# Optimization experiments

Hardware: AMD Instinct MI355X
Metric: run time of the kernel (lower is better)

Reference implementation:

```python
import jax, jax.numpy as jnp
import numpy as np
from jax import lax

B = 8            # IMAGES_PER_GPU
A = 261888       # num_anchors (1024x1024 Mask R-CNN FPN anchors)
PRE_NMS_LIMIT = 6000
PROPOSAL_COUNT = 1000
NMS_THRESHOLD = 0.7


def setup_inputs() -> dict:
    key = jax.random.key(0)
    k1, k2, k3, k4 = jax.random.split(key, 4)
    rpn_probs = jax.random.uniform(k1, (B, A, 2), dtype=jnp.float32)
    rpn_bbox = jax.random.normal(k2, (B, A, 4), dtype=jnp.float32)
    # valid normalized anchors: y1,x1 in [0,0.9], height/width in [0.01,0.1]
    yx = jax.random.uniform(k3, (B, A, 2), minval=0.0, maxval=0.9)
    hw = jax.random.uniform(k4, (B, A, 2), minval=0.01, maxval=0.1)
    anchors = jnp.concatenate([yx, yx + hw], axis=-1)  # (y1, x1, y2, x2)
    return {"rpn_probs": rpn_probs, "rpn_bbox": rpn_bbox, "anchors": anchors}


def _apply_box_deltas(boxes, deltas):
    # boxes, deltas: [..., 4] in (y1, x1, y2, x2) / (dy, dx, log(dh), log(dw))
    h = boxes[..., 2] - boxes[..., 0]
    w = boxes[..., 3] - boxes[..., 1]
    cy = boxes[..., 0] + 0.5 * h + deltas[..., 0] * h
    cx = boxes[..., 1] + 0.5 * w + deltas[..., 1] * w
    h = h * jnp.exp(deltas[..., 2])
    w = w * jnp.exp(deltas[..., 3])
    y1 = cy - 0.5 * h
    x1 = cx - 0.5 * w
    return jnp.stack([y1, x1, y1 + h, x1 + w], axis=-1)


def _nms_single(boxes, scores):
    # boxes: [K, 4] already sorted by score descending; greedy NMS, zero-padded
    areas = (boxes[:, 2] - boxes[:, 0]) * (boxes[:, 3] - boxes[:, 1])

    def step(valid, _):
        idx = jnp.argmax(valid)          # first still-valid = highest score
        has = valid[idx]                 # False when no candidates remain
        box = boxes[idx]
        yy1 = jnp.maximum(box[0], boxes[:, 0])
        xx1 = jnp.maximum(box[1], boxes[:, 1])
        yy2 = jnp.minimum(box[2], boxes[:, 2])
        xx2 = jnp.minimum(box[3], boxes[:, 3])
        inter = jnp.maximum(yy2 - yy1, 0.0) * jnp.maximum(xx2 - xx1, 0.0)
        union = (box[2] - box[0]) * (box[3] - box[1]) + areas - inter
        iou = lax.stop_gradient(jnp.where(union > 0, inter / union, 0.0))
        valid = valid & (iou <= NMS_THRESHOLD)  # also suppresses idx (self IoU = 1)
        return valid, jnp.where(has, box, jnp.zeros_like(box))

    _, selected = lax.scan(step, jnp.ones(boxes.shape[0], dtype=bool), None,
                           length=PROPOSAL_COUNT)
    return selected  # [PROPOSAL_COUNT, 4], zero-padded like tf.pad in original


def reference(rpn_probs, rpn_bbox, anchors):
    std = jnp.asarray([0.1, 0.1, 0.2, 0.2], dtype=rpn_bbox.dtype)  # RPN_BBOX_STD_DEV
    scores = rpn_probs[:, :, 1]                 # fg prob [B, A]
    deltas = rpn_bbox * std
    k = min(PRE_NMS_LIMIT, anchors.shape[1])
    top_scores, ix = lax.top_k(scores, k)       # sorted descending, [B, K]
    idx = ix[..., None]
    deltas_k = jnp.take_along_axis(deltas, idx, axis=1)    # [B, K, 4]
    anchors_k = jnp.take_along_axis(anchors, idx, axis=1)  # [B, K, 4]
    boxes = jnp.clip(_apply_box_deltas(anchors_k, deltas_k), 0.0, 1.0)  # window [0,0,1,1]
    return jax.vmap(_nms_single)(boxes, top_scores)  # [B, PROPOSAL_COUNT, 4]
```

## Files before the change

kernel.cpp:

```cpp
#include <hip/hip_runtime.h>
#include <math.h>
#include <stdint.h>

typedef uint32_t u32; typedef uint64_t u64; typedef uint16_t u16; typedef int32_t i32;

#define BATCH 8
#define NA    261888
#define SEGS  32
#define SEGCHUNK 8184
#define WCHUNK 2046
#define SUBCAP 64
#define NSUB  128
#define TOPK  6000
#define PROP  1000
#define TOP1  1024
#define TMPCAP 2048
#define CACHEB 8192
#define FBMAX 16384
#define NW64  16
#define PSTATIC 0x3F7C0000u

#define OFF_FBK   0
#define OFF_CACHE 1048576
#define OFF_CNT   1572864
#define OFF_STAT  1576960
#define OFF_BOX   1577216
#define OFF_AREA  1708288
#define OFF_MASK  1741056
#define WS_NEEDED 2789632


__device__ __forceinline__ void decode_box(const float4 an, const float4 dl,
                                           float4& bx, float& ar) {
    float d0 = __fmul_rn(dl.x, 0.1f), d1 = __fmul_rn(dl.y, 0.1f);
    float d2 = __fmul_rn(dl.z, 0.2f), d3 = __fmul_rn(dl.w, 0.2f);
    float h = __fsub_rn(an.z, an.x), w = __fsub_rn(an.w, an.y);
    float cy = __fadd_rn(__fadd_rn(an.x, __fmul_rn(0.5f, h)), __fmul_rn(d0, h));
    float cx = __fadd_rn(__fadd_rn(an.y, __fmul_rn(0.5f, w)), __fmul_rn(d1, w));
    float h2 = __fmul_rn(h, (float)exp((double)d2));
    float w2 = __fmul_rn(w, (float)exp((double)d3));
    float y1 = __fsub_rn(cy, __fmul_rn(0.5f, h2));
    float x1 = __fsub_rn(cx, __fmul_rn(0.5f, w2));
    float y2 = __fadd_rn(y1, h2);
    float x2 = __fadd_rn(x1, w2);
    y1 = fminf(fmaxf(y1, 0.f), 1.f); x1 = fminf(fmaxf(x1, 0.f), 1.f);
    y2 = fminf(fmaxf(y2, 0.f), 1.f); x2 = fminf(fmaxf(x2, 0.f), 1.f);
    bx = make_float4(y1, x1, y2, x2);
    ar = __fmul_rn(__fsub_rn(y2, y1), __fsub_rn(x2, x1));
}

__device__ __forceinline__ bool sup_pred(const float4 bi, const float ai,
                                         const float4 bj, const float aj) {
    const double tmid = (double)0.7f + 0x1p-25;
    float yy1 = fmaxf(bi.x, bj.x), xx1 = fmaxf(bi.y, bj.y);
    float yy2 = fminf(bi.z, bj.z), xx2 = fminf(bi.w, bj.w);
    float ih = fmaxf(__fsub_rn(yy2, yy1), 0.f);
    float iw = fmaxf(__fsub_rn(xx2, xx1), 0.f);
    float inter = __fmul_rn(ih, iw);
    float uni = __fsub_rn(__fadd_rn(ai, aj), inter);
    return (uni > 0.f) && ((double)inter >= tmid * (double)uni);
}

__global__ __launch_bounds__(256) void k_histcache(const float4* __restrict__ p4,
                                                   u64* __restrict__ cache,
                                                   u32* __restrict__ cnt) {
    const int b = blockIdx.y, seg = blockIdx.x;
    const int wave = threadIdx.x >> 6, lane = threadIdx.x & 63;
    const u64 lmask = (1ull << lane) - 1ull;
    const size_t fbase = ((size_t)b * NA + seg * SEGCHUNK + wave * WCHUNK) >> 1;
    const u32 abase = (u32)(seg * SEGCHUNK + wave * WCHUNK);
    u64* cseg = cache + (size_t)b * CACHEB + (seg * 4 + wave) * SUBCAP;
    u32 wOff = 0;
    #pragma unroll 4
    for (int it = 0; it < 16; ++it) {
        int f = it * 64 + lane;
        bool ok = f < (WCHUNK / 2);
        u32 bitsA = 0, bitsB = 0;
        if (ok) {
            float4 v = p4[fbase + f];
            bitsA = __float_as_uint(v.y);
            bitsB = __float_as_uint(v.w);
        }
        bool pA = ok && bitsA >= PSTATIC;
        bool pB = ok && bitsB >= PSTATIC;
        u64 mA = __ballot(pA);
        u64 mB = __ballot(pB);
        u32 cA = (u32)__popcll(mA);
        if (pA) {
            u32 slot = wOff + (u32)__popcll(mA & lmask);
            if (slot < SUBCAP) cseg[slot] = ((u64)(~bitsA) << 32) | (u64)(abase + 2 * f);
        }
        if (pB) {
            u32 slot = wOff + cA + (u32)__popcll(mB & lmask);
            if (slot < SUBCAP) cseg[slot] = ((u64)(~bitsB) << 32) | (u64)(abase + 2 * f + 1);
        }
        wOff += cA + (u32)__popcll(mB);
    }
    if (lane == 0) cnt[b * NSUB + seg * 4 + wave] = wOff;
}

__global__ __launch_bounds__(1024) void k_sortdec(const u64* __restrict__ cache,
                                                  const u32* __restrict__ cnt,
                                                  const float4* __restrict__ anchors,
                                                  const float4* __restrict__ bbox,
                                                  u32* __restrict__ stat_g,
                                                  float4* __restrict__ boxes,
                                                  float* __restrict__ areas) {
    __shared__ u32 hist[4096];
    __shared__ u32 suffix[4096];
    __shared__ u32 ps[256];
    __shared__ u32 psS[257];
    __shared__ u64 tmp[TMPCAP];
    __shared__ u32 scnt[NSUB];
    __shared__ u32 wq[4];
    __shared__ u32 sP, sN, sBin, stat;
    const int b = blockIdx.x;
    const int tid = threadIdx.x;
    const int lane = tid & 63, wv = tid >> 6;
    if (tid == 0) { stat = 1u; sBin = 0xFFFFFFFFu; }
    for (int i = tid; i < 4096; i += 1024) hist[i] = 0;
    __syncthreads();
    if (tid < NSUB) {
        u32 raw = cnt[b * NSUB + tid];
        scnt[tid] = raw > SUBCAP ? SUBCAP : raw;
        if (raw > SUBCAP) stat = 0u;
    }
    __syncthreads();
    for (int t = tid; t < CACHEB; t += 1024) {
        int sub = t >> 6, off = t & (SUBCAP - 1);
        if (off < (int)scnt[sub]) {
            u32 bits = ~((u32)(cache[(size_t)b * CACHEB + t] >> 32));
            atomicAdd(&hist[(bits >> 6) & 0xFFFu], 1u);
        }
    }
    __syncthreads();
    if (tid < 256) {
        u32 su = 0;
        #pragma unroll
        for (int k = 0; k < 16; ++k) su += hist[tid * 16 + k];
        ps[tid] = su;
    }
    __syncthreads();
    {
        u32 v = (tid < 256) ? ps[tid] : 0u;
        #pragma unroll
        for (int d = 1; d < 64; d <<= 1) {
            u32 o = __shfl_down(v, d);
            if (lane + d < 64) v += o;
        }
        if (tid < 256 && lane == 0) wq[wv] = v;
        __syncthreads();
        if (tid < 256) {
            u32 add = 0;
            for (int q = wv + 1; q < 4; ++q) add += wq[q];
            psS[tid] = v + add;
        }
        if (tid == 0) psS[256] = 0u;
        __syncthreads();
    }
    {
        const int t4 = tid * 4;
        const int seg = tid >> 2;
        const int segEnd = seg * 16 + 15;
        u32 tail = 0;
        for (int bb = t4 + 4; bb <= segEnd; ++bb) tail += hist[bb];
        u32 h0 = hist[t4], h1 = hist[t4 + 1], h2 = hist[t4 + 2], h3 = hist[t4 + 3];
        u32 s3 = psS[seg + 1] + tail;
        u32 s2 = s3 + h3;
        u32 s1 = s2 + h2;
        u32 s0 = s1 + h1;
        suffix[t4] = s0; suffix[t4 + 1] = s1; suffix[t4 + 2] = s2; suffix[t4 + 3] = s3;
        if (s0 < TOP1 && s0 + h0 >= TOP1) sBin = (u32)t4;
        if (s1 < TOP1 && s1 + h1 >= TOP1) sBin = (u32)(t4 + 1);
        if (s2 < TOP1 && s2 + h2 >= TOP1) sBin = (u32)(t4 + 2);
        if (s3 < TOP1 && s3 + h3 >= TOP1) sBin = (u32)(t4 + 3);
    }
    __syncthreads();
    if (tid == 0) {
        if (sBin == 0xFFFFFFFFu) stat = 0u;
        else {
            sP = PSTATIC + (sBin << 6);
            u32 n = suffix[sBin] + hist[sBin];
            sN = n;
            if (n > TMPCAP) stat = 0u;
        }
    }
    __syncthreads();
    if (stat) {
        for (int i = tid; i < 4096; i += 1024) hist[i] = 0;
        __syncthreads();
        const u32 P = sP;
        for (int t = tid; t < CACHEB; t += 1024) {
            int sub = t >> 6, off = t & (SUBCAP - 1);
            if (off < (int)scnt[sub]) {
                u64 key = cache[(size_t)b * CACHEB + t];
                u32 bits = ~((u32)(key >> 32));
                if (bits >= P) {
                    u32 bin = (bits >> 6) & 0xFFFu;
                    u32 arr = atomicAdd(&hist[bin], 1u);
                    tmp[suffix[bin] + arr] = key;
                }
            }
        }
        __syncthreads();
        const u32 n = sN;
        for (u32 t = (u32)tid; t < n; t += 1024) {
            u64 key = tmp[t];
            u32 bits = ~((u32)(key >> 32));
            u32 bin = (bits >> 6) & 0xFFFu;
            u32 base = suffix[bin], len = hist[bin];
            u32 pos = base;
            for (u32 q = base; q < base + len; ++q) pos += (tmp[q] < key) ? 1u : 0u;
            if (pos < TOP1) {
                u32 idx = (u32)key;
                float4 bx; float ar;
                decode_box(anchors[(size_t)b * NA + idx], bbox[(size_t)b * NA + idx], bx, ar);
                boxes[b * TOP1 + pos] = bx;
                areas[b * TOP1 + pos] = ar;
            }
        }
    }
    if (tid == 0) stat_g[b] = stat;
}

__global__ __launch_bounds__(256) void k_mask(const float4* __restrict__ boxes,
                                              const float* __restrict__ areas,
                                              u32* __restrict__ mw32) {
    const int b = blockIdx.y;
    const int wave = threadIdx.x >> 6, lane = threadIdx.x & 63;
    const int irow = blockIdx.x * 4 + wave;
    const int cmax = irow >> 6;
    u32* mt = mw32 + (size_t)b * (NW64 * TOP1 * 2);
    float4 bi = boxes[b * TOP1 + irow];
    float  ai = areas[b * TOP1 + irow];
    u32 myw = 0;
    for (int c = 0; c <= cmax; ++c) {
        float4 bj = boxes[b * TOP1 + c * 64 + lane];
        float  aj = areas[b * TOP1 + c * 64 + lane];
        u64 word = __ballot(sup_pred(bi, ai, bj, aj));
        if (lane == 2 * c)     myw = (u32)word;
        if (lane == 2 * c + 1) myw = (u32)(word >> 32);
    }
    if (lane < 2 * (cmax + 1))
        mt[((lane >> 1) << 11) + (irow << 1) + (lane & 1)] = myw;
}

__global__ __launch_bounds__(1024, 4) void k_nms(const u64* __restrict__ mw_all,
                                                 const float4* __restrict__ boxes,
                                                 const float2* __restrict__ p2,
                                                 const float4* __restrict__ bbox,
                                                 const float4* __restrict__ anchors,
                                                 const u32* __restrict__ stat_g,
                                                 u64* __restrict__ fbkeys,
                                                 float4* __restrict__ out) {
    __shared__ u64 ldsV[NW64];
    __shared__ u32 wpre[NW64 + 1];
    __shared__ u32 sVt;
    const int b = blockIdx.x;
    const int tid = threadIdx.x;
    const int wave = tid >> 6, lane = tid & 63;
    if (wave == 0) {
        const u64* mw = mw_all + (size_t)b * (NW64 * TOP1);
        const u64 lmask = (1ull << lane) - 1ull;
        u64 V[NW64];
        #pragma unroll
        for (int c = 0; c < NW64; ++c) {
            const int i = (c << 6) + lane;
            u64 ext = 0;
            #pragma unroll
            for (int w = 0; w < c; ++w)
                ext |= mw[(w << 10) + i] & V[w];
            const u64 intern = mw[(c << 10) + i] & lmask;
            const bool extSup = (ext != 0ull);
            u64 v = ~0ull;
            for (int it = 0; it < 64; ++it) {
                bool alive = (!extSup) && ((intern & v) == 0ull);
                u64 nv = __ballot(alive);
                if (nv == v) break;
                v = nv;
            }
            V[c] = v;
        }
        if (lane == 0) {
            u32 r = 0;
            #pragma unroll
            for (int c = 0; c < NW64; ++c) { ldsV[c] = V[c]; wpre[c] = r; r += (u32)__popcll(V[c]); }
            wpre[NW64] = r; sVt = r;
        }
    }
    __syncthreads();
    const u32 Vt = sVt;
    if (Vt >= PROP && stat_g[b] != 0u) {
        const int i = tid;
        const int w = i >> 6, bit = i & 63;
        u64 vw = ldsV[w];
        bool isv = ((vw >> bit) & 1ull) != 0ull;
        u32 rank = wpre[w] + (u32)__popcll(vw & ((1ull << bit) - 1ull));
        if (isv && rank < PROP) out[b * PROP + rank] = boxes[b * TOP1 + i];
        return;
    }
    const int i = tid;
    __shared__ float4 abox[PROP];
    __shared__ float  aar[PROP];
    __shared__ u32 fh[4096];
    __shared__ u32 fps[256];
    __shared__ u32 nsh, sP6;
    if (i == 0) nsh = 0;
    for (int z = i; z < 4096; z += 1024) fh[z] = 0;
    __syncthreads();
    for (int a = i; a < NA; a += 1024) {
        u32 bits = __float_as_uint(p2[(size_t)b * NA + a].y);
        atomicAdd(&fh[bits >> 18], 1u);
    }
    __syncthreads();
    if (i < 256) {
        u32 su = 0;
        for (int k = 0; k < 16; ++k) su += fh[i * 16 + k];
        fps[i] = su;
    }
    __syncthreads();
    if (i == 0) {
        u32 acc = 0; int seg = 0;
        for (int t = 255; t >= 0; --t) { if (acc + fps[t] >= TOPK) { seg = t; break; } acc += fps[t]; }
        int b6 = seg * 16; u32 g6 = acc;
        for (int k = 15; k >= 0; --k) {
            u32 c = fh[seg * 16 + k];
            if (g6 + c >= TOPK) { b6 = seg * 16 + k; break; }
            g6 += c;
        }
        sP6 = (u32)b6 << 18;
    }
    __syncthreads();
    u32 P6 = sP6;
    for (int a = i; a < NA; a += 1024) {
        u32 bits = __float_as_uint(p2[(size_t)b * NA + a].y);
        if (bits >= P6) {
            u32 p = atomicAdd(&nsh, 1u);
            if (p < FBMAX) fbkeys[(size_t)b * FBMAX + p] = ((u64)(~bits) << 32) | (u64)a;
        }
    }
    __syncthreads();
    u32 n = nsh; if (n > FBMAX) n = FBMAX;
    volatile u64* vk = (volatile u64*)(fbkeys + (size_t)b * FBMAX);
    for (int i2 = (int)n + i; i2 < FBMAX; i2 += 1024) vk[i2] = ~0ull;
    __syncthreads();
    for (int k = 2; k <= FBMAX; k <<= 1) {
        for (int j = k >> 1; j > 0; j >>= 1) {
            for (int p = i; p < FBMAX / 2; p += 1024) {
                int ii = ((p & ~(j - 1)) << 1) | (p & (j - 1));
                int l = ii | j;
                u64 a = vk[ii], c = vk[l];
                bool up = ((ii & k) == 0);
                if ((a > c) == up) { vk[ii] = c; vk[l] = a; }
            }
            __syncthreads();
        }
    }
    int acc_n = 0;
    int limit = (int)n < TOPK ? (int)n : TOPK;
    for (int t = 0; t < limit && acc_n < PROP; ++t) {
        u32 idx = (u32)vk[t];
        float4 bi2; float ai2;
        decode_box(anchors[(size_t)b * NA + idx], bbox[(size_t)b * NA + idx], bi2, ai2);
        int pred = 0;
        if (i < acc_n) pred = sup_pred(bi2, ai2, abox[i], aar[i]) ? 1 : 0;
        int any = __syncthreads_or(pred);
        if (!any) {
            if (i == 0) {
                abox[acc_n] = bi2; aar[acc_n] = ai2;
                out[b * PROP + acc_n] = bi2;
            }
            ++acc_n;
            __syncthreads();
        }
    }
    for (int t = acc_n + i; t < PROP; t += 1024)
        out[b * PROP + t] = make_float4(0.f, 0.f, 0.f, 0.f);
}


extern "C" void kernel_launch(void* const* d_in, const int* in_sizes, int n_in,
                              void* d_out, int out_size, void* d_ws, size_t ws_size,
                              hipStream_t stream) {
    (void)in_sizes; (void)n_in; (void)out_size;
    if (ws_size < (size_t)WS_NEEDED) return;
    const float2* p2      = (const float2*)d_in[0];
    const float4* p4      = (const float4*)d_in[0];
    const float4* bbox    = (const float4*)d_in[1];
    const float4* anchors = (const float4*)d_in[2];
    float4* out = (float4*)d_out;

    char* ws = (char*)d_ws;
    u64* fbkeys  = (u64*)(ws + OFF_FBK);
    u64* cache   = (u64*)(ws + OFF_CACHE);
    u32* cnt     = (u32*)(ws + OFF_CNT);
    u32* stat_g  = (u32*)(ws + OFF_STAT);
    float4* boxes= (float4*)(ws + OFF_BOX);
    float* areas = (float*)(ws + OFF_AREA);
    u32* mw32    = (u32*)(ws + OFF_MASK);
    u64* mw64    = (u64*)(ws + OFF_MASK);

    dim3 ghc(SEGS, BATCH), gmask(TOP1 / 4, BATCH);
    k_histcache<<<ghc,   256, 0, stream>>>(p4, cache, cnt);
    k_sortdec  <<<BATCH, 1024, 0, stream>>>(cache, cnt, anchors, bbox, stat_g, boxes, areas);
    k_mask     <<<gmask, 256, 0, stream>>>(boxes, areas, mw32);
    k_nms      <<<BATCH, 1024, 0, stream>>>(mw64, boxes, p2, bbox, anchors, stat_g, fbkeys, out);
}
```

Before: 141.6 us.

## Fuse IoU mask and NMS kernels via last-block-done atomic counter

Merges the suppression-mask kernel and the greedy NMS kernel into one launch. Each 1024-thread block computes 16 mask rows, then increments a per-image atomic counter, and the last block to finish per image runs the NMS. This removes one kernel launch and the gap between launches. In exchange it adds threadfence and atomic synchronisation, plus a reset of the counter in the first kernel. It also fully unrolls the histogram loop.

Measured after the change: 164.1 us. 1.16x slower.

```diff
diff --git a/kernel.cpp b/kernel.cpp
--- a/kernel.cpp
+++ b/kernel.cpp
@@ -18,12 +18,14 @@
 #define CACHEB 8192
 #define FBMAX 16384
 #define NW64  16
+#define MBLK  64
 #define PSTATIC 0x3F7C0000u
 
 #define OFF_FBK   0
 #define OFF_CACHE 1048576
 #define OFF_CNT   1572864
 #define OFF_STAT  1576960
+#define OFF_DONE  1577088
 #define OFF_BOX   1577216
 #define OFF_AREA  1708288
 #define OFF_MASK  1741056
@@ -63,15 +65,17 @@
 
 __global__ __launch_bounds__(256) void k_histcache(const float4* __restrict__ p4,
                                                    u64* __restrict__ cache,
-                                                   u32* __restrict__ cnt) {
+                                                   u32* __restrict__ cnt,
+                                                   u32* __restrict__ done) {
     const int b = blockIdx.y, seg = blockIdx.x;
     const int wave = threadIdx.x >> 6, lane = threadIdx.x & 63;
+    if (seg == 0 && b == 0 && threadIdx.x < BATCH) done[threadIdx.x] = 0;
     const u64 lmask = (1ull << lane) - 1ull;
     const size_t fbase = ((size_t)b * NA + seg * SEGCHUNK + wave * WCHUNK) >> 1;
     const u32 abase = (u32)(seg * SEGCHUNK + wave * WCHUNK);
     u64* cseg = cache + (size_t)b * CACHEB + (seg * 4 + wave) * SUBCAP;
     u32 wOff = 0;
-    #pragma unroll 4
+    #pragma unroll
     for (int it = 0; it < 16; ++it) {
         int f = it * 64 + lane;
         bool ok = f < (WCHUNK / 2);
@@ -223,44 +227,51 @@
     if (tid == 0) stat_g[b] = stat;
 }
 
-__global__ __launch_bounds__(256) void k_mask(const float4* __restrict__ boxes,
-                                              const float* __restrict__ areas,
-                                              u32* __restrict__ mw32) {
-    const int b = blockIdx.y;
-    const int wave = threadIdx.x >> 6, lane = threadIdx.x & 63;
-    const int irow = blockIdx.x * 4 + wave;
-    const int cmax = irow >> 6;
-    u32* mt = mw32 + (size_t)b * (NW64 * TOP1 * 2);
-    float4 bi = boxes[b * TOP1 + irow];
-    float  ai = areas[b * TOP1 + irow];
-    u32 myw = 0;
-    for (int c = 0; c <= cmax; ++c) {
-        float4 bj = boxes[b * TOP1 + c * 64 + lane];
-        float  aj = areas[b * TOP1 + c * 64 + lane];
-        u64 word = __ballot(sup_pred(bi, ai, bj, aj));
-        if (lane == 2 * c)     myw = (u32)word;
-        if (lane == 2 * c + 1) myw = (u32)(word >> 32);
-    }
-    if (lane < 2 * (cmax + 1))
-        mt[((lane >> 1) << 11) + (irow << 1) + (lane & 1)] = myw;
-}
-
-__global__ __launch_bounds__(1024, 4) void k_nms(const u64* __restrict__ mw_all,
-                                                 const float4* __restrict__ boxes,
-                                                 const float2* __restrict__ p2,
-                                                 const float4* __restrict__ bbox,
-                                                 const float4* __restrict__ anchors,
-                                                 const u32* __restrict__ stat_g,
-                                                 u64* __restrict__ fbkeys,
-                                                 float4* __restrict__ out) {
+__global__ __launch_bounds__(1024) void k_masknms(const float4* __restrict__ boxes,
+                                                  const float* __restrict__ areas,
+                                                  const float2* __restrict__ p2,
+                                                  const float4* __restrict__ bbox,
+                                                  const float4* __restrict__ anchors,
+                                                  const u32* __restrict__ stat_g,
+                                                  u32* __restrict__ done,
+                                                  u32* __restrict__ mw32,
+                                                  const u64* __restrict__ mw64,
+                                                  u64* __restrict__ fbkeys,
+                                                  float4* __restrict__ out) {
     __shared__ u64 ldsV[NW64];
     __shared__ u32 wpre[NW64 + 1];
-    __shared__ u32 sVt;
-    const int b = blockIdx.x;
+    __shared__ u32 sWin, sVt;
+    const int b = blockIdx.y;
     const int tid = threadIdx.x;
     const int wave = tid >> 6, lane = tid & 63;
+    {
+        const int irow = blockIdx.x * 16 + wave;
+        const int cmax = irow >> 6;
+        u32* mt = mw32 + (size_t)b * (NW64 * TOP1 * 2);
+        float4 bi = boxes[b * TOP1 + irow];
+        float  ai = areas[b * TOP1 + irow];
+        u32 myw = 0;
+        for (int c = 0; c <= cmax; ++c) {
+            float4 bj = boxes[b * TOP1 + c * 64 + lane];
+            float  aj = areas[b * TOP1 + c * 64 + lane];
+            u64 word = __ballot(sup_pred(bi, ai, bj, aj));
+            if (lane == 2 * c)     myw = (u32)word;
+            if (lane == 2 * c + 1) myw = (u32)(word >> 32);
+        }
+        if (lane < 2 * (cmax + 1))
+            mt[((lane >> 1) << 11) + (irow << 1) + (lane & 1)] = myw;
+    }
+    __syncthreads();
+    if (tid == 0) {
+        __threadfence();
+        u32 old = atomicAdd(&done[b], 1u);
+        sWin = (old == (u32)(MBLK - 1)) ? 1u : 0u;
+    }
+    __syncthreads();
+    if (!sWin) return;
+    __threadfence();
     if (wave == 0) {
-        const u64* mw = mw_all + (size_t)b * (NW64 * TOP1);
+        const u64* mw = mw64 + (size_t)b * (NW64 * TOP1);
         const u64 lmask = (1ull << lane) - 1ull;
         u64 V[NW64];
         #pragma unroll
@@ -395,14 +406,14 @@
     u64* cache   = (u64*)(ws + OFF_CACHE);
     u32* cnt     = (u32*)(ws + OFF_CNT);
     u32* stat_g  = (u32*)(ws + OFF_STAT);
+    u32* done    = (u32*)(ws + OFF_DONE);
     float4* boxes= (float4*)(ws + OFF_BOX);
     float* areas = (float*)(ws + OFF_AREA);
     u32* mw32    = (u32*)(ws + OFF_MASK);
     u64* mw64    = (u64*)(ws + OFF_MASK);
 
-    dim3 ghc(SEGS, BATCH), gmask(TOP1 / 4, BATCH);
-    k_histcache<<<ghc,   256, 0, stream>>>(p4, cache, cnt);
+    dim3 ghc(SEGS, BATCH), gmn(MBLK, BATCH);
+    k_histcache<<<ghc,   256, 0, stream>>>(p4, cache, cnt, done);
     k_sortdec  <<<BATCH, 1024, 0, stream>>>(cache, cnt, anchors, bbox, stat_g, boxes, areas);
-    k_mask     <<<gmask, 256, 0, stream>>>(boxes, areas, mw32);
-    k_nms      <<<BATCH, 1024, 0, stream>>>(mw64, boxes, p2, bbox, anchors, stat_g, fbkeys, out);
-}
+    k_masknms  <<<gmn,  1024, 0, stream>>>(boxes, areas, p2, bbox, anchors, stat_g, done, mw32, mw64, fbkeys, out);
+}
```

## Spread NMS bitmask resolution across all 16 waves with per-chunk barriers

Applied to the files above, without the earlier changes.

The serial single-wave greedy NMS over 16 chunks of 64 candidates is split so that each wave owns one 64-row chunk. Each wave preloads its suppression-mask rows into registers up front and accumulates external suppression as earlier chunks finalise, with a block barrier between chunks. This removes the 120 dependent global loads on one wave's critical path, at the cost of 16 block-wide syncs. The histogram loop is also fully unrolled.

Result: faster. 135.6 us, median of 2 (-4.2%).

```diff
diff --git a/kernel.cpp b/kernel.cpp
--- a/kernel.cpp
+++ b/kernel.cpp
@@ -71,7 +71,7 @@
     const u32 abase = (u32)(seg * SEGCHUNK + wave * WCHUNK);
     u64* cseg = cache + (size_t)b * CACHEB + (seg * 4 + wave) * SUBCAP;
     u32 wOff = 0;
-    #pragma unroll 4
+    #pragma unroll
     for (int it = 0; it < 16; ++it) {
         int f = it * 64 + lane;
         bool ok = f < (WCHUNK / 2);
@@ -255,41 +255,47 @@
                                                  float4* __restrict__ out) {
     __shared__ u64 ldsV[NW64];
     __shared__ u32 wpre[NW64 + 1];
-    __shared__ u32 sVt;
     const int b = blockIdx.x;
     const int tid = threadIdx.x;
     const int wave = tid >> 6, lane = tid & 63;
-    if (wave == 0) {
+    {
         const u64* mw = mw_all + (size_t)b * (NW64 * TOP1);
         const u64 lmask = (1ull << lane) - 1ull;
-        u64 V[NW64];
+        u64 rr[NW64];
+        u64 intern = 0;
         #pragma unroll
-        for (int c = 0; c < NW64; ++c) {
-            const int i = (c << 6) + lane;
-            u64 ext = 0;
-            #pragma unroll
-            for (int w = 0; w < c; ++w)
-                ext |= mw[(w << 10) + i] & V[w];
-            const u64 intern = mw[(c << 10) + i] & lmask;
-            const bool extSup = (ext != 0ull);
-            u64 v = ~0ull;
-            for (int it = 0; it < 64; ++it) {
-                bool alive = (!extSup) && ((intern & v) == 0ull);
-                u64 nv = __ballot(alive);
-                if (nv == v) break;
-                v = nv;
+        for (int w = 0; w < NW64; ++w) {
+            u64 v = 0;
+            if (w <= wave) v = mw[(w << 10) + (wave << 6) + lane];
+            if (w == wave) intern = v & lmask;
+            rr[w] = (w < wave) ? v : 0ull;
+        }
+        u64 ext = 0;
+        #pragma unroll
+        for (int s = 0; s < NW64; ++s) {
+            if (wave == s) {
+                const bool extSup = (ext != 0ull);
+                u64 v = ~0ull;
+                for (int it = 0; it < 64; ++it) {
+                    bool alive = (!extSup) && ((intern & v) == 0ull);
+                    u64 nv = __ballot(alive);
+                    if (nv == v) break;
+                    v = nv;
+                }
+                if (lane == 0) ldsV[s] = v;
             }
-            V[c] = v;
-        }
-        if (lane == 0) {
-            u32 r = 0;
-            #pragma unroll
-            for (int c = 0; c < NW64; ++c) { ldsV[c] = V[c]; wpre[c] = r; r += (u32)__popcll(V[c]); }
-            wpre[NW64] = r; sVt = r;
-        }
-    }
-    __syncthreads();
-    const u32 Vt = sVt;
+            __syncthreads();
+            if (wave > s) ext |= rr[s] & ldsV[s];
+        }
+    }
+    if (tid == 0) {
+        u32 r = 0;
+        #pragma unroll
+        for (int c = 0; c < NW64; ++c) { wpre[c] = r; r += (u32)__popcll(ldsV[c]); }
+        wpre[NW64] = r;
+    }
+    __syncthreads();
+    const u32 Vt = wpre[NW64];
     if (Vt >= PROP && stat_g[b] != 0u) {
         const int i = tid;
         const int w = i >> 6, bit = i & 63;
```
